# Optimization experiments

Measured on AMD Instinct MI355X. Metric: run time of the kernel, lower is better.

The kernel has to match this reference:

```python
import jax, jax.numpy as jnp
import numpy as np

B, T, P, H1, H2 = 4096, 64, 64, 512, 512
EPS = 1e-3  # bn_eps


def _bn(x, g, b):
    # x: [B, T, D]; g, b: [T, D]. Training-mode BatchNorm1d: batch stats over B,
    # biased variance (divide by N), per (timestep, feature).
    m = jnp.mean(x, axis=0)                      # [T, D]
    v = jnp.mean((x - m) ** 2, axis=0)           # [T, D]
    return (x - m) * jax.lax.rsqrt(v + EPS) * g + b


def setup_inputs() -> dict:
    key = jax.random.key(0)
    ks = jax.random.split(key, 8)
    prices = jax.random.normal(ks[0], (B, T, P), dtype=jnp.float32)
    W1 = jax.random.normal(ks[1], (T, P, H1), dtype=jnp.float32) / np.sqrt(P)
    b1 = jax.random.normal(ks[2], (T, H1), dtype=jnp.float32) * 0.01
    W2 = jax.random.normal(ks[3], (T, H1, H2), dtype=jnp.float32) / np.sqrt(H1)
    b2 = jax.random.normal(ks[4], (T, H2), dtype=jnp.float32) * 0.01
    W3 = jax.random.normal(ks[5], (T, H2, P), dtype=jnp.float32) / np.sqrt(H2)
    b3 = jax.random.normal(ks[6], (T, P), dtype=jnp.float32) * 0.01
    return {
        "prices": prices,
        "bn0_g": jnp.ones((T, P), jnp.float32), "bn0_b": jnp.zeros((T, P), jnp.float32),
        "W1": W1, "b1": b1,
        "bn1_g": jnp.ones((T, H1), jnp.float32), "bn1_b": jnp.zeros((T, H1), jnp.float32),
        "W2": W2, "b2": b2,
        "bn2_g": jnp.ones((T, H2), jnp.float32), "bn2_b": jnp.zeros((T, H2), jnp.float32),
        "W3": W3, "b3": b3,
    }


def reference(prices, bn0_g, bn0_b, W1, b1, bn1_g, bn1_b, W2, b2, bn2_g, bn2_b, W3, b3):
    # Per-timestep: BN -> Linear -> BN -> ReLU -> Linear -> BN -> ReLU -> Linear,
    # with distinct weights per step, vectorized over T via batched einsums.
    x = _bn(prices, bn0_g, bn0_b)                          # [B, T, P]
    h = jnp.einsum('btp,tph->bth', x, W1) + b1             # [B, T, H1]
    h = jax.nn.relu(_bn(h, bn1_g, bn1_b))
    h = jnp.einsum('bth,thk->btk', h, W2) + b2             # [B, T, H2]
    h = jax.nn.relu(_bn(h, bn2_g, bn2_b))
    out = jnp.einsum('btk,tkp->btp', h, W3) + b3           # [B, T, P]
    return out
```

## Files before the change

### kernel.cpp

```cpp
#include <hip/hip_runtime.h>
#include <hip/hip_bf16.h>


#define B_ 4096
#define T_ 64
#define P_ 64
#define H1_ 512
#define H2_ 512
#define TC_ 8
#define BN_EPS 1e-3f

typedef float f32x4 __attribute__((ext_vector_type(4)));
typedef short s16x8 __attribute__((ext_vector_type(8)));
typedef unsigned short u16;
typedef unsigned short u16x8 __attribute__((ext_vector_type(8)));

__device__ __forceinline__ u16 f2bf(float f) {
  union { float f; unsigned u; } x; x.f = f;
  unsigned r = x.u + 0x7fffu + ((x.u >> 16) & 1u);
  return (u16)(r >> 16);
}
__device__ __forceinline__ float bf2f(u16 h) {
  union { unsigned u; float f; } x; x.u = ((unsigned)h) << 16;
  return x.f;
}

__global__ void stats0_k(const float* __restrict__ x, float* __restrict__ sum,
                         float* __restrict__ sq) {
  const int t = blockIdx.x;
  const int chunk = blockIdx.y;
  const int tid = threadIdx.x;
  const int p = tid & 63;
  const int bs = tid >> 6;
  float s = 0.f, q = 0.f;
  const int b0 = chunk * (B_ / 8), bend = b0 + (B_ / 8);
  for (int b = b0 + bs; b < bend; b += 4) {
    float v = x[((size_t)b * T_ + t) * P_ + p];
    s += v; q += v * v;
  }
  __shared__ float ls[4][64], lq[4][64];
  ls[bs][p] = s; lq[bs][p] = q;
  __syncthreads();
  if (tid < 64) {
    float S = ls[0][tid] + ls[1][tid] + ls[2][tid] + ls[3][tid];
    float Q = lq[0][tid] + lq[1][tid] + lq[2][tid] + lq[3][tid];
    atomicAdd(&sum[t * P_ + tid], S);
    atomicAdd(&sq[t * P_ + tid], Q);
  }
}

__global__ void finalize_k(const float* __restrict__ sum, const float* __restrict__ sq,
                           const float* __restrict__ g, const float* __restrict__ b,
                           float* __restrict__ s, float* __restrict__ sh, int n) {
  int i = blockIdx.x * 256 + threadIdx.x;
  if (i >= n) return;
  float m = sum[i] * (1.f / B_);
  float v = sq[i] * (1.f / B_) - m * m;
  float sc = g[i] * rsqrtf(v + BN_EPS);
  s[i] = sc;
  sh[i] = b[i] - m * sc;
}

__global__ void fold1_k(const float* __restrict__ W1, const float* __restrict__ b1,
                        const float* __restrict__ s0, const float* __restrict__ sh0,
                        u16* __restrict__ W1t, float* __restrict__ b1p) {
  const int t = blockIdx.x;
  const int h = blockIdx.y * 256 + threadIdx.x;
  float acc = b1[t * H1_ + h];
  for (int p = 0; p < P_; ++p) {
    float w = W1[((size_t)t * P_ + p) * H1_ + h];
    acc += sh0[t * P_ + p] * w;
    W1t[((size_t)t * H1_ + h) * P_ + p] = f2bf(w * s0[t * P_ + p]);
  }
  b1p[t * H1_ + h] = acc;
}

template <int KD, int ND>
__global__ void castWT_k(const float* __restrict__ W, u16* __restrict__ Wt) {
  const int t = blockIdx.z;
  const int kb = blockIdx.y * 64;
  const int nb = blockIdx.x * 64;
  __shared__ float tile[64][65];
  const int tid = threadIdx.x;
  {
    const int n = tid & 63, k0 = tid >> 6;
    for (int i = k0; i < 64; i += 4)
      tile[i][n] = W[((size_t)t * KD + kb + i) * ND + nb + n];
  }
  __syncthreads();
  {
    const int k = tid & 63, n0 = tid >> 6;
    for (int j = n0; j < 64; j += 4)
      Wt[((size_t)t * ND + nb + j) * KD + kb + k] = f2bf(tile[k][j]);
  }
}

template <int K_DIM, int N_DIM, int BM, int BN, int BK, int WM, int WN,
          int TA, int TO, bool A_F32, bool PRE_BN, bool STATS, bool OUT_F32,
          bool A_LOCAL, bool O_LOCAL>
__global__ __launch_bounds__(256) void gemm_k(
    const void* __restrict__ Av, const u16* __restrict__ Bt,
    const float* __restrict__ bias,
    const float* __restrict__ bsum, const float* __restrict__ bsq,
    const float* __restrict__ bg, const float* __restrict__ bb,
    void* __restrict__ Out, float* __restrict__ osum, float* __restrict__ osq,
    int t0) {
  constexpr int GX = N_DIM / BN;
  constexpr int WTM = BM / WM, WTN = BN / WN;
  constexpr int FM = WTM / 16, FN = WTN / 16;
  constexpr int LDK = BK + 8;
  constexpr int ACH = BM * BK / 8 / 256;
  constexpr int BCH = BN * BK / 8 / 256;
  __shared__ __align__(16) u16 As[BM][LDK];
  __shared__ __align__(16) u16 Bs[BN][LDK];
  __shared__ __align__(16) float sS[PRE_BN ? K_DIM : 4];
  __shared__ __align__(16) float sH[PRE_BN ? K_DIM : 4];

  const int bid = blockIdx.x;
  const int tz = bid % TC_;
  const int jj = bid / TC_;
  const int bx = jj % GX, by = jj / GX;
  const int tg = t0 + tz;
  const int ta = A_LOCAL ? tz : tg;
  const int to = O_LOCAL ? tz : tg;
  const int brow0 = by * BM;
  const int bcol0 = bx * BN;
  const int tid = threadIdx.x;
  const int lane = tid & 63;
  const int wid = tid >> 6;
  const int wm = wid / WN, wn = wid % WN;

  if constexpr (PRE_BN) {
    for (int i = tid; i < K_DIM; i += 256) {
      const float m = bsum[(size_t)tg * K_DIM + i] * (1.f / B_);
      const float v = bsq[(size_t)tg * K_DIM + i] * (1.f / B_) - m * m;
      const float sc = bg[(size_t)tg * K_DIM + i] * rsqrtf(v + BN_EPS);
      sS[i] = sc;
      sH[i] = bb[(size_t)tg * K_DIM + i] - m * sc;
    }
    __syncthreads();
  }

  f32x4 acc[FM][FN] = {};
  u16x8 pa[A_F32 ? 1 : ACH];
  float4 paf[A_F32 ? 2 * ACH : 1];
  u16x8 pb[BCH];

  auto loadT = [&](int k0) {
#pragma unroll
    for (int i = 0; i < ACH; ++i) {
      const int c = tid + i * 256;
      const int row = c / (BK / 8), col = (c % (BK / 8)) * 8;
      const size_t goff = ((size_t)(brow0 + row) * TA + ta) * K_DIM + k0 + col;
      if constexpr (A_F32) {
        const float* src = (const float*)Av + goff;
        paf[2 * i] = *(const float4*)src;
        paf[2 * i + 1] = *(const float4*)(src + 4);
      } else {
        pa[i] = *(const u16x8*)((const u16*)Av + goff);
      }
    }
#pragma unroll
    for (int i = 0; i < BCH; ++i) {
      const int c = tid + i * 256;
      const int row = c / (BK / 8), col = (c % (BK / 8)) * 8;
      pb[i] = *(const u16x8*)(Bt +
               ((size_t)tg * N_DIM + bcol0 + row) * K_DIM + k0 + col);
    }
  };

  auto writeT = [&](int k0) {
#pragma unroll
    for (int i = 0; i < ACH; ++i) {
      const int c = tid + i * 256;
      const int row = c / (BK / 8), col = (c % (BK / 8)) * 8;
      u16x8 v;
      if constexpr (A_F32) {
        const float fv[8] = {paf[2*i].x, paf[2*i].y, paf[2*i].z, paf[2*i].w,
                             paf[2*i+1].x, paf[2*i+1].y, paf[2*i+1].z, paf[2*i+1].w};
#pragma unroll
        for (int q = 0; q < 8; ++q) v[q] = f2bf(fv[q]);
      } else if constexpr (PRE_BN) {
        const float4 s0v = *(const float4*)&sS[k0 + col];
        const float4 s1v = *(const float4*)&sS[k0 + col + 4];
        const float4 h0v = *(const float4*)&sH[k0 + col];
        const float4 h1v = *(const float4*)&sH[k0 + col + 4];
        const float ss[8] = {s0v.x, s0v.y, s0v.z, s0v.w, s1v.x, s1v.y, s1v.z, s1v.w};
        const float hh[8] = {h0v.x, h0v.y, h0v.z, h0v.w, h1v.x, h1v.y, h1v.z, h1v.w};
#pragma unroll
        for (int q = 0; q < 8; ++q)
          v[q] = f2bf(fmaxf(bf2f(pa[i][q]) * ss[q] + hh[q], 0.f));
      } else {
        v = pa[i];
      }
      *(u16x8*)&As[row][col] = v;
    }
#pragma unroll
    for (int i = 0; i < BCH; ++i) {
      const int c = tid + i * 256;
      const int row = c / (BK / 8), col = (c % (BK / 8)) * 8;
      *(u16x8*)&Bs[row][col] = pb[i];
    }
  };

  loadT(0);
  for (int k0 = 0; k0 < K_DIM; k0 += BK) {
    writeT(k0);
    __syncthreads();
    if (k0 + BK < K_DIM) loadT(k0 + BK);
#pragma unroll
    for (int ks = 0; ks < BK / 32; ++ks) {
      s16x8 aF[FM], bF[FN];
#pragma unroll
      for (int m = 0; m < FM; ++m)
        aF[m] = *(const s16x8*)&As[wm * WTM + m * 16 + (lane & 15)]
                                  [ks * 32 + (lane >> 4) * 8];
#pragma unroll
      for (int n = 0; n < FN; ++n)
        bF[n] = *(const s16x8*)&Bs[wn * WTN + n * 16 + (lane & 15)]
                                  [ks * 32 + (lane >> 4) * 8];
#pragma unroll
      for (int m = 0; m < FM; ++m)
#pragma unroll
        for (int n = 0; n < FN; ++n)
          acc[m][n] = __builtin_amdgcn_mfma_f32_16x16x32_bf16(aF[m], bF[n],
                                                              acc[m][n], 0, 0, 0);
    }
    __syncthreads();
  }

  const int r0 = (lane >> 4) * 4;
  const int cl = lane & 15;
#pragma unroll
  for (int n = 0; n < FN; ++n) {
    const int ncol = bcol0 + wn * WTN + n * 16 + cl;
    const float bv = bias[(size_t)tg * N_DIM + ncol];
    float csum = 0.f, csq = 0.f;
#pragma unroll
    for (int m = 0; m < FM; ++m) {
      const int rbase = brow0 + wm * WTM + m * 16 + r0;
#pragma unroll
      for (int r = 0; r < 4; ++r) {
        const float h = acc[m][n][r] + bv;
        if constexpr (STATS) { csum += h; csq += h * h; }
        const size_t oidx = ((size_t)(rbase + r) * TO + to) * N_DIM + ncol;
        if constexpr (OUT_F32) ((float*)Out)[oidx] = h;
        else                   ((u16*)Out)[oidx] = f2bf(h);
      }
    }
    if constexpr (STATS) {
      csum += __shfl_xor(csum, 16);
      csum += __shfl_xor(csum, 32);
      csq += __shfl_xor(csq, 16);
      csq += __shfl_xor(csq, 32);
      if (lane < 16) {
        atomicAdd(&osum[(size_t)tg * N_DIM + ncol], csum);
        atomicAdd(&osq[(size_t)tg * N_DIM + ncol], csq);
      }
    }
  }
}

extern "C" void kernel_launch(void* const* d_in, const int* in_sizes, int n_in,
                              void* d_out, int out_size, void* d_ws, size_t ws_size,
                              hipStream_t stream) {
  const float* prices = (const float*)d_in[0];
  const float* bn0_g = (const float*)d_in[1];
  const float* bn0_b = (const float*)d_in[2];
  const float* W1 = (const float*)d_in[3];
  const float* b1 = (const float*)d_in[4];
  const float* bn1_g = (const float*)d_in[5];
  const float* bn1_b = (const float*)d_in[6];
  const float* W2 = (const float*)d_in[7];
  const float* b2 = (const float*)d_in[8];
  const float* bn2_g = (const float*)d_in[9];
  const float* bn2_b = (const float*)d_in[10];
  const float* W3 = (const float*)d_in[11];
  const float* b3 = (const float*)d_in[12];
  (void)in_sizes; (void)n_in; (void)out_size;

  if (ws_size < 115343360ull) return;

  char* ws = (char*)d_ws;
  size_t off = 0;
  auto alloc = [&](size_t bytes) -> void* {
    void* p = ws + off;
    off += (bytes + 255) & ~(size_t)255;
    return p;
  };
  float* sum0 = (float*)alloc(T_ * P_ * 4);
  float* sq0 = (float*)alloc(T_ * P_ * 4);
  float* sum1 = (float*)alloc(T_ * H1_ * 4);
  float* sq1 = (float*)alloc(T_ * H1_ * 4);
  float* sum2 = (float*)alloc(T_ * H2_ * 4);
  float* sq2 = (float*)alloc(T_ * H2_ * 4);
  const size_t statsBytes = off;
  float* s0 = (float*)alloc(T_ * P_ * 4);
  float* sh0 = (float*)alloc(T_ * P_ * 4);
  float* b1p = (float*)alloc(T_ * H1_ * 4);
  u16* W1t = (u16*)alloc((size_t)T_ * H1_ * P_ * 2);
  u16* W2t = (u16*)alloc((size_t)T_ * H1_ * H2_ * 2);
  u16* W3t = (u16*)alloc((size_t)T_ * H2_ * P_ * 2);
  u16* h1c = (u16*)alloc((size_t)B_ * TC_ * H1_ * 2);
  u16* h2c = (u16*)alloc((size_t)B_ * TC_ * H2_ * 2);

  hipMemsetAsync(d_ws, 0, statsBytes, stream);

  stats0_k<<<dim3(T_, 8), 256, 0, stream>>>(prices, sum0, sq0);
  finalize_k<<<(T_ * P_ + 255) / 256, 256, 0, stream>>>(sum0, sq0, bn0_g, bn0_b,
                                                        s0, sh0, T_ * P_);
  fold1_k<<<dim3(T_, H1_ / 256), 256, 0, stream>>>(W1, b1, s0, sh0, W1t, b1p);
  castWT_k<H1_, H2_><<<dim3(H2_ / 64, H1_ / 64, T_), 256, 0, stream>>>(W2, W2t);
  castWT_k<H2_, P_><<<dim3(P_ / 64, H2_ / 64, T_), 256, 0, stream>>>(W3, W3t);

  for (int c = 0; c < T_ / TC_; ++c) {
    const int t0 = c * TC_;
    gemm_k<P_, H1_, 128, 128, 64, 2, 2, T_, TC_, true, false, true, false, false, true>
        <<<(H1_ / 128) * (B_ / 128) * TC_, 256, 0, stream>>>(
            prices, W1t, b1p, nullptr, nullptr, nullptr, nullptr,
            h1c, sum1, sq1, t0);
    gemm_k<H1_, H2_, 128, 128, 64, 2, 2, TC_, TC_, false, true, true, false, true, true>
        <<<(H2_ / 128) * (B_ / 128) * TC_, 256, 0, stream>>>(
            h1c, W2t, b2, sum1, sq1, bn1_g, bn1_b, h2c, sum2, sq2, t0);
    gemm_k<H2_, P_, 64, 64, 64, 2, 2, TC_, T_, false, true, false, true, true, false>
        <<<(P_ / 64) * (B_ / 64) * TC_, 256, 0, stream>>>(
            h2c, W3t, b3, sum2, sq2, bn2_g, bn2_b, d_out, nullptr, nullptr, t0);
  }
}
```

Before: 834.3 us.

## Stream B tiles via direct global-to-LDS loads with XOR-swizzled double-buffered LDS

The GEMM kernel now loads weight tiles straight from global memory into LDS with global_load_lds, double-buffered so the next tile is fetched during the current MFMA loop. The padded LDS layout is replaced by an XOR swizzle, applied to both A and B, to avoid bank conflicts. Separately, the BN0 stats kernel is rewritten as a vectorized row-sweep, and the finalize kernel is folded into fold1_k, which drops one launch. These aim to cut register staging and VGPR pressure for B, and to reduce preprocessing overhead. The cost is more LDS (two B buffers) and reliance on correct swizzle and wait semantics for the async LDS loads.

New measurement: 762.5 us. 8.6% less time.

```diff
diff --git a/kernel.cpp b/kernel.cpp
--- a/kernel.cpp
+++ b/kernel.cpp
@@ -1,5 +1,6 @@
 #include <hip/hip_runtime.h>
 #include <hip/hip_bf16.h>
+#include <stdint.h>
 
 
 #define B_ 4096
@@ -25,52 +26,58 @@
   return x.f;
 }
 
+__device__ __forceinline__ void gl2lds16(const u16* g, u16* l) {
+  auto gp = reinterpret_cast<const __attribute__((address_space(1))) uint32_t*>(
+      reinterpret_cast<uintptr_t>(g));
+  auto lp = reinterpret_cast<__attribute__((address_space(3))) uint32_t*>(
+      reinterpret_cast<uintptr_t>(l));
+  __builtin_amdgcn_global_load_lds(gp, lp, 16, 0, 0);
+}
+
+__device__ __forceinline__ int swz(int row, int colbyte) {
+  return (row << 6) + ((colbyte ^ ((row & 7) << 4)) >> 1);
+}
+
 __global__ void stats0_k(const float* __restrict__ x, float* __restrict__ sum,
                          float* __restrict__ sq) {
-  const int t = blockIdx.x;
-  const int chunk = blockIdx.y;
-  const int tid = threadIdx.x;
-  const int p = tid & 63;
-  const int bs = tid >> 6;
-  float s = 0.f, q = 0.f;
-  const int b0 = chunk * (B_ / 8), bend = b0 + (B_ / 8);
-  for (int b = b0 + bs; b < bend; b += 4) {
-    float v = x[((size_t)b * T_ + t) * P_ + p];
-    s += v; q += v * v;
-  }
-  __shared__ float ls[4][64], lq[4][64];
-  ls[bs][p] = s; lq[bs][p] = q;
-  __syncthreads();
-  if (tid < 64) {
-    float S = ls[0][tid] + ls[1][tid] + ls[2][tid] + ls[3][tid];
-    float Q = lq[0][tid] + lq[1][tid] + lq[2][tid] + lq[3][tid];
-    atomicAdd(&sum[t * P_ + tid], S);
-    atomicAdd(&sq[t * P_ + tid], Q);
-  }
-}
-
-__global__ void finalize_k(const float* __restrict__ sum, const float* __restrict__ sq,
-                           const float* __restrict__ g, const float* __restrict__ b,
-                           float* __restrict__ s, float* __restrict__ sh, int n) {
-  int i = blockIdx.x * 256 + threadIdx.x;
-  if (i >= n) return;
-  float m = sum[i] * (1.f / B_);
-  float v = sq[i] * (1.f / B_) - m * m;
-  float sc = g[i] * rsqrtf(v + BN_EPS);
-  s[i] = sc;
-  sh[i] = b[i] - m * sc;
+  const int col4 = blockIdx.x * 256 + threadIdx.x;
+  const int r0 = blockIdx.y * 64;
+  const float* src = x + (size_t)r0 * (T_ * P_) + col4 * 4;
+  f32x4 s = {0.f, 0.f, 0.f, 0.f}, q = {0.f, 0.f, 0.f, 0.f};
+#pragma unroll 4
+  for (int r = 0; r < 64; ++r) {
+    const f32x4 v = *(const f32x4*)(src + (size_t)r * (T_ * P_));
+    s += v;
+    q += v * v;
+  }
+#pragma unroll
+  for (int j = 0; j < 4; ++j) {
+    atomicAdd(&sum[col4 * 4 + j], s[j]);
+    atomicAdd(&sq[col4 * 4 + j], q[j]);
+  }
 }
 
 __global__ void fold1_k(const float* __restrict__ W1, const float* __restrict__ b1,
-                        const float* __restrict__ s0, const float* __restrict__ sh0,
+                        const float* __restrict__ sum0, const float* __restrict__ sq0,
+                        const float* __restrict__ g0, const float* __restrict__ bb0,
                         u16* __restrict__ W1t, float* __restrict__ b1p) {
   const int t = blockIdx.x;
-  const int h = blockIdx.y * 256 + threadIdx.x;
+  const int tid = threadIdx.x;
+  __shared__ float s0l[P_], sh0l[P_];
+  if (tid < P_) {
+    const float m = sum0[t * P_ + tid] * (1.f / B_);
+    const float v = sq0[t * P_ + tid] * (1.f / B_) - m * m;
+    const float sc = g0[t * P_ + tid] * rsqrtf(v + BN_EPS);
+    s0l[tid] = sc;
+    sh0l[tid] = bb0[t * P_ + tid] - m * sc;
+  }
+  __syncthreads();
+  const int h = blockIdx.y * 256 + tid;
   float acc = b1[t * H1_ + h];
   for (int p = 0; p < P_; ++p) {
-    float w = W1[((size_t)t * P_ + p) * H1_ + h];
-    acc += sh0[t * P_ + p] * w;
-    W1t[((size_t)t * H1_ + h) * P_ + p] = f2bf(w * s0[t * P_ + p]);
+    const float w = W1[((size_t)t * P_ + p) * H1_ + h];
+    acc += sh0l[p] * w;
+    W1t[((size_t)t * H1_ + h) * P_ + p] = f2bf(w * s0l[p]);
   }
   b1p[t * H1_ + h] = acc;
 }
@@ -95,7 +102,7 @@
   }
 }
 
-template <int K_DIM, int N_DIM, int BM, int BN, int BK, int WM, int WN,
+template <int K_DIM, int N_DIM, int BM, int BN, int WM, int WN,
           int TA, int TO, bool A_F32, bool PRE_BN, bool STATS, bool OUT_F32,
           bool A_LOCAL, bool O_LOCAL>
 __global__ __launch_bounds__(256) void gemm_k(
@@ -105,14 +112,14 @@
     const float* __restrict__ bg, const float* __restrict__ bb,
     void* __restrict__ Out, float* __restrict__ osum, float* __restrict__ osq,
     int t0) {
+  constexpr int BK = 64;
   constexpr int GX = N_DIM / BN;
   constexpr int WTM = BM / WM, WTN = BN / WN;
   constexpr int FM = WTM / 16, FN = WTN / 16;
-  constexpr int LDK = BK + 8;
-  constexpr int ACH = BM * BK / 8 / 256;
-  constexpr int BCH = BN * BK / 8 / 256;
-  __shared__ __align__(16) u16 As[BM][LDK];
-  __shared__ __align__(16) u16 Bs[BN][LDK];
+  constexpr int ACH = BM * 8 / 256;
+  constexpr int NCH = BN * 128 / 1024;
+  __shared__ __align__(16) u16 AsL[BM * 64];
+  __shared__ __align__(16) u16 BsL[2][BN * 64];
   __shared__ __align__(16) float sS[PRE_BN ? K_DIM : 4];
   __shared__ __align__(16) float sH[PRE_BN ? K_DIM : 4];
 
@@ -144,13 +151,12 @@
   f32x4 acc[FM][FN] = {};
   u16x8 pa[A_F32 ? 1 : ACH];
   float4 paf[A_F32 ? 2 * ACH : 1];
-  u16x8 pb[BCH];
-
-  auto loadT = [&](int k0) {
+
+  auto loadA = [&](int k0) {
 #pragma unroll
     for (int i = 0; i < ACH; ++i) {
       const int c = tid + i * 256;
-      const int row = c / (BK / 8), col = (c % (BK / 8)) * 8;
+      const int row = c >> 3, col = (c & 7) * 8;
       const size_t goff = ((size_t)(brow0 + row) * TA + ta) * K_DIM + k0 + col;
       if constexpr (A_F32) {
         const float* src = (const float*)Av + goff;
@@ -160,20 +166,25 @@
         pa[i] = *(const u16x8*)((const u16*)Av + goff);
       }
     }
-#pragma unroll
-    for (int i = 0; i < BCH; ++i) {
-      const int c = tid + i * 256;
-      const int row = c / (BK / 8), col = (c % (BK / 8)) * 8;
-      pb[i] = *(const u16x8*)(Bt +
-               ((size_t)tg * N_DIM + bcol0 + row) * K_DIM + k0 + col);
-    }
   };
 
-  auto writeT = [&](int k0) {
+  const int rsub = lane >> 3;
+  const int koffB = ((lane & 7) ^ rsub) * 8;
+  auto issueB = [&](int k0, int buf) {
+    const u16* gbase =
+        Bt + ((size_t)tg * N_DIM + bcol0) * K_DIM + k0 + koffB;
+#pragma unroll
+    for (int ch = wid; ch < NCH; ch += 4) {
+      const u16* g = gbase + (size_t)(ch * 8 + rsub) * K_DIM;
+      gl2lds16(g, &BsL[buf][ch * 512]);
+    }
+  };
+
+  auto writeA = [&](int k0) {
 #pragma unroll
     for (int i = 0; i < ACH; ++i) {
       const int c = tid + i * 256;
-      const int row = c / (BK / 8), col = (c % (BK / 8)) * 8;
+      const int row = c >> 3, colb = (c & 7) * 16;
       u16x8 v;
       if constexpr (A_F32) {
         const float fv[8] = {paf[2*i].x, paf[2*i].y, paf[2*i].z, paf[2*i].w,
@@ -181,10 +192,11 @@
 #pragma unroll
         for (int q = 0; q < 8; ++q) v[q] = f2bf(fv[q]);
       } else if constexpr (PRE_BN) {
-        const float4 s0v = *(const float4*)&sS[k0 + col];
-        const float4 s1v = *(const float4*)&sS[k0 + col + 4];
-        const float4 h0v = *(const float4*)&sH[k0 + col];
-        const float4 h1v = *(const float4*)&sH[k0 + col + 4];
+        const int col = k0 + (c & 7) * 8;
+        const float4 s0v = *(const float4*)&sS[col];
+        const float4 s1v = *(const float4*)&sS[col + 4];
+        const float4 h0v = *(const float4*)&sH[col];
+        const float4 h1v = *(const float4*)&sH[col + 4];
         const float ss[8] = {s0v.x, s0v.y, s0v.z, s0v.w, s1v.x, s1v.y, s1v.z, s1v.w};
         const float hh[8] = {h0v.x, h0v.y, h0v.z, h0v.w, h1v.x, h1v.y, h1v.z, h1v.w};
 #pragma unroll
@@ -193,32 +205,33 @@
       } else {
         v = pa[i];
       }
-      *(u16x8*)&As[row][col] = v;
-    }
-#pragma unroll
-    for (int i = 0; i < BCH; ++i) {
-      const int c = tid + i * 256;
-      const int row = c / (BK / 8), col = (c % (BK / 8)) * 8;
-      *(u16x8*)&Bs[row][col] = pb[i];
+      *(u16x8*)&AsL[swz(row, colb)] = v;
     }
   };
 
-  loadT(0);
+  loadA(0);
+  issueB(0, 0);
+  int cur = 0;
   for (int k0 = 0; k0 < K_DIM; k0 += BK) {
-    writeT(k0);
+    writeA(k0);
     __syncthreads();
-    if (k0 + BK < K_DIM) loadT(k0 + BK);
-#pragma unroll
-    for (int ks = 0; ks < BK / 32; ++ks) {
+    if (k0 + BK < K_DIM) {
+      loadA(k0 + BK);
+      issueB(k0 + BK, cur ^ 1);
+    }
+#pragma unroll
+    for (int ks = 0; ks < 2; ++ks) {
       s16x8 aF[FM], bF[FN];
 #pragma unroll
-      for (int m = 0; m < FM; ++m)
-        aF[m] = *(const s16x8*)&As[wm * WTM + m * 16 + (lane & 15)]
-                                  [ks * 32 + (lane >> 4) * 8];
-#pragma unroll
-      for (int n = 0; n < FN; ++n)
-        bF[n] = *(const s16x8*)&Bs[wn * WTN + n * 16 + (lane & 15)]
-                                  [ks * 32 + (lane >> 4) * 8];
+      for (int m = 0; m < FM; ++m) {
+        const int row = wm * WTM + m * 16 + (lane & 15);
+        aF[m] = *(const s16x8*)&AsL[swz(row, ks * 64 + ((lane >> 4) << 4))];
+      }
+#pragma unroll
+      for (int n = 0; n < FN; ++n) {
+        const int row = wn * WTN + n * 16 + (lane & 15);
+        bF[n] = *(const s16x8*)&BsL[cur][swz(row, ks * 64 + ((lane >> 4) << 4))];
+      }
 #pragma unroll
       for (int m = 0; m < FM; ++m)
 #pragma unroll
@@ -227,6 +240,7 @@
                                                               acc[m][n], 0, 0, 0);
     }
     __syncthreads();
+    cur ^= 1;
   }
 
   const int r0 = (lane >> 4) * 4;
@@ -295,8 +309,6 @@
   float* sum2 = (float*)alloc(T_ * H2_ * 4);
   float* sq2 = (float*)alloc(T_ * H2_ * 4);
   const size_t statsBytes = off;
-  float* s0 = (float*)alloc(T_ * P_ * 4);
-  float* sh0 = (float*)alloc(T_ * P_ * 4);
   float* b1p = (float*)alloc(T_ * H1_ * 4);
   u16* W1t = (u16*)alloc((size_t)T_ * H1_ * P_ * 2);
   u16* W2t = (u16*)alloc((size_t)T_ * H1_ * H2_ * 2);
@@ -304,25 +316,24 @@
   u16* h1c = (u16*)alloc((size_t)B_ * TC_ * H1_ * 2);
   u16* h2c = (u16*)alloc((size_t)B_ * TC_ * H2_ * 2);
 
-  hipMemsetAsync(d_ws, 0, statsBytes, stream);
-
-  stats0_k<<<dim3(T_, 8), 256, 0, stream>>>(prices, sum0, sq0);
-  finalize_k<<<(T_ * P_ + 255) / 256, 256, 0, stream>>>(sum0, sq0, bn0_g, bn0_b,
-                                                        s0, sh0, T_ * P_);
-  fold1_k<<<dim3(T_, H1_ / 256), 256, 0, stream>>>(W1, b1, s0, sh0, W1t, b1p);
+  (void)hipMemsetAsync(d_ws, 0, statsBytes, stream);
+
+  stats0_k<<<dim3(4, 64), 256, 0, stream>>>(prices, sum0, sq0);
+  fold1_k<<<dim3(T_, H1_ / 256), 256, 0, stream>>>(W1, b1, sum0, sq0,
+                                                   bn0_g, bn0_b, W1t, b1p);
   castWT_k<H1_, H2_><<<dim3(H2_ / 64, H1_ / 64, T_), 256, 0, stream>>>(W2, W2t);
   castWT_k<H2_, P_><<<dim3(P_ / 64, H2_ / 64, T_), 256, 0, stream>>>(W3, W3t);
 
   for (int c = 0; c < T_ / TC_; ++c) {
     const int t0 = c * TC_;
-    gemm_k<P_, H1_, 128, 128, 64, 2, 2, T_, TC_, true, false, true, false, false, true>
+    gemm_k<P_, H1_, 128, 128, 2, 2, T_, TC_, true, false, true, false, false, true>
         <<<(H1_ / 128) * (B_ / 128) * TC_, 256, 0, stream>>>(
             prices, W1t, b1p, nullptr, nullptr, nullptr, nullptr,
             h1c, sum1, sq1, t0);
-    gemm_k<H1_, H2_, 128, 128, 64, 2, 2, TC_, TC_, false, true, true, false, true, true>
+    gemm_k<H1_, H2_, 128, 128, 2, 2, TC_, TC_, false, true, true, false, true, true>
         <<<(H2_ / 128) * (B_ / 128) * TC_, 256, 0, stream>>>(
             h1c, W2t, b2, sum1, sq1, bn1_g, bn1_b, h2c, sum2, sq2, t0);
-    gemm_k<H2_, P_, 64, 64, 64, 2, 2, TC_, T_, false, true, false, true, true, false>
+    gemm_k<H2_, P_, 64, 64, 2, 2, TC_, T_, false, true, false, true, true, false>
         <<<(P_ / 64) * (B_ / 64) * TC_, 256, 0, stream>>>(
             h2c, W3t, b3, sum2, sq2, bn2_g, bn2_b, d_out, nullptr, nullptr, t0);
   }
```
